# Performance work log

Hardware: AMD Instinct MI355X
Metric: run time of the kernel (lower is better)

The kernel has to match this reference:

```python
import jax, jax.numpy as jnp
import numpy as np

HIDDEN = 2048
N_HEADS = 16
HEAD_DIM = HIDDEN // N_HEADS
INV_NORM = 1.0 / float(np.sqrt(HEAD_DIM))
BETA = 1.0


def setup_inputs() -> dict:
    key = jax.random.key(0)
    ks = jax.random.split(key, 12)
    B, S, H = 2, 2048, HIDDEN
    scale = 1.0 / float(np.sqrt(H))
    return {
        "hidden_states": jax.random.normal(ks[0], (B, S, H), jnp.float32),
        "residual": jax.random.normal(ks[1], (B, S, H), jnp.float32),
        "alibi": jax.random.normal(ks[2], (B * N_HEADS, 1, S), jnp.float32),
        "Wq": jax.random.normal(ks[3], (H, H), jnp.float32) * scale,
        "bq": jnp.zeros((H,), jnp.float32),
        "Wk": jax.random.normal(ks[4], (H, H), jnp.float32) * scale,
        "bk": jnp.zeros((H,), jnp.float32),
        "Wv": jax.random.normal(ks[5], (H, H), jnp.float32) * scale,
        "bv": jnp.zeros((H,), jnp.float32),
        "Wd": jax.random.normal(ks[6], (H, H), jnp.float32) * scale,
        "bd": jnp.zeros((H,), jnp.float32),
    }


def reference(hidden_states, residual, alibi, Wq, bq, Wk, bk, Wv, bv, Wd, bd):
    B, S, H = hidden_states.shape
    # separate QKV projections (nn.Linear: x @ W^T + b)
    q = hidden_states @ Wq.T + bq
    k = hidden_states @ Wk.T + bk
    v = hidden_states @ Wv.T + bv
    # [B, n_heads, S, head_dim]
    q = q.reshape(B, S, N_HEADS, HEAD_DIM).transpose(0, 2, 1, 3)
    k = k.reshape(B, S, N_HEADS, HEAD_DIM).transpose(0, 2, 1, 3)
    v = v.reshape(B, S, N_HEADS, HEAD_DIM).transpose(0, 2, 1, 3)
    # baddbmm: scores = beta * alibi + inv_norm * q @ k^T, per (batch*head)
    alibi_bh = alibi.reshape(B, N_HEADS, 1, S)  # broadcasts over query dim
    scores = BETA * alibi_bh + INV_NORM * jnp.einsum("bhqd,bhkd->bhqk", q, k)
    probs = jax.nn.softmax(scores.astype(jnp.float32), axis=-1).astype(v.dtype)
    # attention dropout: p=0.0 (identity)
    ctx = jnp.einsum("bhqk,bhkd->bhqd", probs, v)  # [B,H,S,D]
    ctx = ctx.transpose(0, 2, 1, 3).reshape(B, S, H)
    out = ctx @ Wd.T + bd
    # hidden dropout p=0.0 then residual add (dropout_add)
    return out + residual
```

## Files before the change

kernel.cpp:

```cpp
#include <hip/hip_runtime.h>

#define HID   2048
#define NHEAD 16
#define HD    128
#define SEQ   2048
#define BATCH 2
#define MROWS (BATCH*SEQ)
#define NQKV  (3*HID)
#define INV_NORM 0.08838834764831845f
#define LOG2E    1.4426950408889634f
#define SCALE_L2 (INV_NORM*LOG2E)

typedef __attribute__((ext_vector_type(8)))  __bf16 bf16x8;
typedef __attribute__((ext_vector_type(4)))  float  f32x4;
typedef __attribute__((ext_vector_type(16))) float  f32x16;

typedef __attribute__((address_space(1))) void GV;
typedef __attribute__((address_space(3))) void LV;

__device__ __forceinline__ void async16(const void* g, void* l) {
  __builtin_amdgcn_global_load_lds((const GV*)g, (LV*)l, 16, 0, 0);
}

__device__ __forceinline__ unsigned short f2bf(float f) {
  unsigned u = __builtin_bit_cast(unsigned, f);
  u += 0x7FFFu + ((u >> 16) & 1u);
  return (unsigned short)(u >> 16);
}

__device__ __forceinline__ unsigned pkbf(float a, float b) {
#if __has_builtin(__builtin_amdgcn_cvt_pk_bf16_f32)
  typedef __attribute__((ext_vector_type(2))) __bf16 bf16x2;
  bf16x2 r = __builtin_amdgcn_cvt_pk_bf16_f32(a, b);
  return __builtin_bit_cast(unsigned, r);
#else
  return (unsigned)f2bf(a) | ((unsigned)f2bf(b) << 16);
#endif
}

__device__ __forceinline__ void mfma16(f32x4& c, bf16x8 a, bf16x8 b) {
  c = __builtin_amdgcn_mfma_f32_16x16x32_bf16(a, b, c, 0, 0, 0);
}

__global__ __launch_bounds__(256) void cvt_kernel(const float* __restrict__ src,
                                                  unsigned short* __restrict__ dst, int n) {
  int i = (blockIdx.x * 256 + threadIdx.x) * 4;
  if (i >= n) return;
  float4 v = *(const float4*)(src + i);
  ushort4 o;
  o.x = f2bf(v.x); o.y = f2bf(v.y); o.z = f2bf(v.z); o.w = f2bf(v.w);
  *(ushort4*)(dst + i) = o;
}

__global__ __launch_bounds__(256) void cvtw_kernel(const float* __restrict__ W0,
                                                   const float* __restrict__ W1,
                                                   const float* __restrict__ W2,
                                                   const float* __restrict__ W3,
                                                   unsigned short* __restrict__ dst) {
  int sel = blockIdx.y;
  const float* src = (sel == 0) ? W0 : (sel == 1) ? W1 : (sel == 2) ? W2 : W3;
  unsigned short* d = dst + (size_t)sel * HID * HID;
  int i = (blockIdx.x * 256 + threadIdx.x) * 4;
  float4 v = *(const float4*)(src + i);
  ushort4 o;
  o.x = f2bf(v.x); o.y = f2bf(v.y); o.z = f2bf(v.z); o.w = f2bf(v.w);
  *(ushort4*)(d + i) = o;
}

__device__ __forceinline__ void gemm_core(const unsigned short* __restrict__ A,
                                          const unsigned short* __restrict__ Bm,
                                          int K, int m0, int n0,
                                          unsigned short* As, unsigned short* Bs,
                                          f32x4 (&acc)[4][4]) {
  const int tid  = threadIdx.x;
  const int w    = tid >> 6;
  const int lane = tid & 63;
  const int l16  = lane & 15;
  const int quad = lane >> 4;
  const int wm   = (w & 1) * 64;
  const int wn   = (w >> 1) * 64;

  const f32x4 zero = {0.f, 0.f, 0.f, 0.f};
#pragma unroll
  for (int i = 0; i < 4; ++i)
#pragma unroll
    for (int j = 0; j < 4; ++j) acc[i][j] = zero;

  for (int k0 = 0; k0 < K; k0 += 64) {
    __syncthreads();
#pragma unroll
    for (int i = 0; i < 4; ++i) {
      int slot = i * 256 + w * 64 + lane;
      int r = slot >> 3;
      int c = (slot & 7) ^ (r & 7);
      async16(A  + (size_t)(m0 + r) * K + k0 + c * 8, (char*)As + (size_t)(i * 256 + w * 64) * 16);
      async16(Bm + (size_t)(n0 + r) * K + k0 + c * 8, (char*)Bs + (size_t)(i * 256 + w * 64) * 16);
    }
    __syncthreads();

#pragma unroll
    for (int kk = 0; kk < 2; ++kk) {
      bf16x8 af[4], bfp[4];
#pragma unroll
      for (int i = 0; i < 4; ++i) {
        int rr = wm + i * 16 + l16;
        af[i] = *(const bf16x8*)(As + ((rr * 8 + (((kk * 4 + quad)) ^ (rr & 7))) * 8));
      }
#pragma unroll
      for (int j = 0; j < 4; ++j) {
        int rr = wn + j * 16 + l16;
        bfp[j] = *(const bf16x8*)(Bs + ((rr * 8 + (((kk * 4 + quad)) ^ (rr & 7))) * 8));
      }
#pragma unroll
      for (int i = 0; i < 4; ++i)
#pragma unroll
        for (int j = 0; j < 4; ++j) mfma16(acc[i][j], af[i], bfp[j]);
    }
  }
}

__global__ __launch_bounds__(256) void gemm_qkv_kernel(
    const unsigned short* __restrict__ Xb, const unsigned short* __restrict__ Wb,
    const float* __restrict__ bq, const float* __restrict__ bk,
    const float* __restrict__ bv, unsigned short* __restrict__ Cout) {
  __shared__ __align__(16) unsigned short As[128 * 64];
  __shared__ __align__(16) unsigned short Bs[128 * 64];
  f32x4 acc[4][4];
  const int m0 = blockIdx.y * 128, n0 = blockIdx.x * 128;
  gemm_core(Xb, Wb, HID, m0, n0, As, Bs, acc);

  const int tid = threadIdx.x, w = tid >> 6, lane = tid & 63;
  const int l16 = lane & 15, quad = lane >> 4;
  const int wm = (w & 1) * 64, wn = (w >> 1) * 64;
#pragma unroll
  for (int j = 0; j < 4; ++j) {
    int ng = n0 + wn + j * 16 + l16;
    float bias = (ng < HID) ? bq[ng] : (ng < 2 * HID ? bk[ng - HID] : bv[ng - 2 * HID]);
#pragma unroll
    for (int i = 0; i < 4; ++i)
#pragma unroll
      for (int r = 0; r < 4; ++r) {
        int mg = m0 + wm + i * 16 + quad * 4 + r;
        Cout[(size_t)mg * NQKV + ng] = f2bf(acc[i][j][r] + bias);
      }
  }
}

__global__ __launch_bounds__(256) void gemm_out_kernel(
    const unsigned short* __restrict__ Ctx, const unsigned short* __restrict__ Wdb,
    const float* __restrict__ bd, const float* __restrict__ Res,
    float* __restrict__ Out) {
  __shared__ __align__(16) unsigned short As[128 * 64];
  __shared__ __align__(16) unsigned short Bs[128 * 64];
  f32x4 acc[4][4];
  const int m0 = blockIdx.y * 128, n0 = blockIdx.x * 128;
  gemm_core(Ctx, Wdb, HID, m0, n0, As, Bs, acc);

  const int tid = threadIdx.x, w = tid >> 6, lane = tid & 63;
  const int l16 = lane & 15, quad = lane >> 4;
  const int wm = (w & 1) * 64, wn = (w >> 1) * 64;
#pragma unroll
  for (int j = 0; j < 4; ++j) {
    int ng = n0 + wn + j * 16 + l16;
    float bias = bd[ng];
#pragma unroll
    for (int i = 0; i < 4; ++i)
#pragma unroll
      for (int r = 0; r < 4; ++r) {
        int mg = m0 + wm + i * 16 + quad * 4 + r;
        size_t off = (size_t)mg * HID + ng;
        Out[off] = acc[i][j][r] + bias + Res[off];
      }
  }
}

__global__ __launch_bounds__(256) void vtrans_kernel(const unsigned short* __restrict__ QKV,
                                                     unsigned short* __restrict__ Vt) {
  __shared__ __align__(16) unsigned short T[64][72];
  const int s0 = blockIdx.x * 64, d0 = blockIdx.y * 64, bh = blockIdx.z;
  const int b = bh >> 4, h = bh & 15;
  const int tid = threadIdx.x;
#pragma unroll
  for (int i = 0; i < 2; ++i) {
    int idx = i * 256 + tid;
    int r = idx >> 3, ch = idx & 7;
    const unsigned short* g = QKV + ((size_t)b * SEQ + s0 + r) * NQKV + 2 * HID + h * HD + d0 + ch * 8;
    *(uint4*)(&T[r][ch * 8]) = *(const uint4*)g;
  }
  __syncthreads();
#pragma unroll
  for (int i = 0; i < 2; ++i) {
    int idx = i * 256 + tid;
    int d = idx >> 3, ch = idx & 7;
    unsigned short v[8];
#pragma unroll
    for (int x = 0; x < 8; ++x) v[x] = T[ch * 8 + x][d];
    unsigned short* g = Vt + ((size_t)bh * HD + d0 + d) * SEQ + s0 + ch * 8;
    *(uint4*)g = *(const uint4*)v;
  }
}

__global__ __launch_bounds__(256, 2) void attn_kernel(
    const unsigned short* __restrict__ QKV, const unsigned short* __restrict__ Vt,
    const float* __restrict__ alibi, unsigned short* __restrict__ Ctx) {
  __shared__ __align__(16) char smem[51200];
  unsigned short* Ks  = (unsigned short*)smem;
  unsigned short* Vts = (unsigned short*)(smem + 16384);
  unsigned short* Ps  = (unsigned short*)(smem + 32768);
  unsigned short* Qs  = (unsigned short*)smem;

  const int tid = threadIdx.x, w = tid >> 6, lane = tid & 63;
  const int l32 = lane & 31, h = lane >> 5;
  const int q0 = blockIdx.x * 128;
  const int bh = blockIdx.y, b = bh >> 4, hh = bh & 15;
  const size_t rowbase = (size_t)b * SEQ;
  const float* ali = alibi + (size_t)bh * SEQ;
  const unsigned short* Vbh = Vt + (size_t)bh * HD * SEQ;

  {
    const unsigned short* qbase = QKV + (rowbase + q0) * NQKV + hh * HD;
#pragma unroll
    for (int i = 0; i < 8; ++i) {
      int slot = i * 256 + w * 64 + lane;
      int r = slot >> 4, c = (slot & 15) ^ (r & 15);
      async16(qbase + (size_t)r * NQKV + c * 8, (char*)Qs + (size_t)(i * 256 + w * 64) * 16);
    }
  }
  __syncthreads();
  bf16x8 qf[8];
  {
    int qr = w * 32 + l32;
#pragma unroll
    for (int ks = 0; ks < 8; ++ks) {
      int c = (ks * 2 + h) ^ (qr & 15);
      qf[ks] = *(const bf16x8*)(Qs + (qr * 16 + c) * 8);
    }
  }

  f32x16 oacc[4];
  float l_acc = 0.f;
#pragma unroll
  for (int nb = 0; nb < 4; ++nb)
#pragma unroll
    for (int r = 0; r < 16; ++r) oacc[nb][r] = 0.f;

  __syncthreads();

  for (int kt = 0; kt < SEQ / 64; ++kt) {
    {
      const unsigned short* kbase = QKV + (rowbase + kt * 64) * NQKV + HID + hh * HD;
#pragma unroll
      for (int i = 0; i < 4; ++i) {
        int slot = i * 256 + w * 64 + lane;
        int r = slot >> 4, c = (slot & 15) ^ (r & 15);
        async16(kbase + (size_t)r * NQKV + c * 8, (char*)Ks + (size_t)(i * 256 + w * 64) * 16);
      }
      const unsigned short* vbase = Vbh + kt * 64;
#pragma unroll
      for (int i = 0; i < 4; ++i) {
        int slot = i * 256 + w * 64 + lane;
        int r = slot >> 3, c = (slot & 7) ^ (r & 7);
        async16(vbase + (size_t)r * SEQ + c * 8, (char*)Vts + (size_t)(i * 256 + w * 64) * 16);
      }
    }
    __syncthreads();

    f32x16 sacc[2];
#pragma unroll
    for (int mb = 0; mb < 2; ++mb)
#pragma unroll
      for (int r = 0; r < 16; ++r) sacc[mb][r] = 0.f;
#pragma unroll
    for (int ks = 0; ks < 8; ++ks) {
      int c = (ks * 2 + h) ^ (l32 & 15);
#pragma unroll
      for (int mb = 0; mb < 2; ++mb) {
        bf16x8 kf = *(const bf16x8*)(Ks + ((mb * 32 + l32) * 16 + ((ks * 2 + h) ^ (l32 & 15))) * 8);
        sacc[mb] = __builtin_amdgcn_mfma_f32_32x32x16_bf16(kf, qf[ks], sacc[mb], 0, 0, 0);
      }
      (void)c;
    }

    const float* alik = ali + kt * 64 + 4 * h;
    const int qrow = w * 32 + l32;
#pragma unroll
    for (int mb = 0; mb < 2; ++mb) {
#pragma unroll
      for (int g = 0; g < 4; ++g) {
        float4 av = *(const float4*)(alik + mb * 32 + g * 8);
        float p0 = __builtin_amdgcn_exp2f(sacc[mb][g * 4 + 0] * SCALE_L2 + av.x * LOG2E);
        float p1 = __builtin_amdgcn_exp2f(sacc[mb][g * 4 + 1] * SCALE_L2 + av.y * LOG2E);
        float p2 = __builtin_amdgcn_exp2f(sacc[mb][g * 4 + 2] * SCALE_L2 + av.z * LOG2E);
        float p3 = __builtin_amdgcn_exp2f(sacc[mb][g * 4 + 3] * SCALE_L2 + av.w * LOG2E);
        l_acc += (p0 + p1) + (p2 + p3);
        uint2 pk;
        pk.x = pkbf(p0, p1);
        pk.y = pkbf(p2, p3);
        *(uint2*)(Ps + qrow * 72 + mb * 32 + g * 8 + 4 * h) = pk;
      }
    }

#pragma unroll
    for (int ks2 = 0; ks2 < 4; ++ks2) {
      bf16x8 pf = *(const bf16x8*)(Ps + qrow * 72 + ks2 * 16 + h * 8);
#pragma unroll
      for (int nb = 0; nb < 4; ++nb) {
        bf16x8 vf = *(const bf16x8*)(Vts + ((nb * 32 + l32) * 8 + ((ks2 * 2 + h) ^ (l32 & 7))) * 8);
        oacc[nb] = __builtin_amdgcn_mfma_f32_32x32x16_bf16(pf, vf, oacc[nb], 0, 0, 0);
      }
    }
    __syncthreads();
  }

  float lf = l_acc + __shfl_xor(l_acc, 32, 64);
  float rinv[16];
#pragma unroll
  for (int reg = 0; reg < 16; ++reg) {
    int row = (reg & 3) + 8 * (reg >> 2) + 4 * h;
    rinv[reg] = 1.0f / __shfl(lf, row, 64);
  }

#pragma unroll
  for (int nb = 0; nb < 4; ++nb)
#pragma unroll
    for (int reg = 0; reg < 16; ++reg) {
      int row = (reg & 3) + 8 * (reg >> 2) + 4 * h;
      size_t qg = rowbase + q0 + w * 32 + row;
      Ctx[qg * HID + hh * HD + nb * 32 + l32] = f2bf(oacc[nb][reg] * rinv[reg]);
    }
}

extern "C" void kernel_launch(void* const* d_in, const int* in_sizes, int n_in,
                              void* d_out, int out_size, void* d_ws, size_t ws_size,
                              hipStream_t stream) {
  const float* hidden   = (const float*)d_in[0];
  const float* residual = (const float*)d_in[1];
  const float* alibi    = (const float*)d_in[2];
  const float* Wq = (const float*)d_in[3];
  const float* bq = (const float*)d_in[4];
  const float* Wk = (const float*)d_in[5];
  const float* bk = (const float*)d_in[6];
  const float* Wv = (const float*)d_in[7];
  const float* bv = (const float*)d_in[8];
  const float* Wd = (const float*)d_in[9];
  const float* bd = (const float*)d_in[10];
  float* out = (float*)d_out;

  unsigned short* Xb    = (unsigned short*)d_ws;
  unsigned short* Wqkvb = Xb + (size_t)MROWS * HID;
  unsigned short* Wdb   = Wqkvb + (size_t)NQKV * HID;
  unsigned short* QKVb  = Wdb + (size_t)HID * HID;
  unsigned short* Ctxb  = QKVb + (size_t)MROWS * NQKV;
  unsigned short* Vtb   = Wqkvb;

  const int nX = MROWS * HID, nW = HID * HID;
  cvt_kernel<<<nX / 4 / 256, 256, 0, stream>>>(hidden, Xb, nX);
  cvtw_kernel<<<dim3(nW / 4 / 256, 4), 256, 0, stream>>>(Wq, Wk, Wv, Wd, Wqkvb);

  gemm_qkv_kernel<<<dim3(NQKV / 128, MROWS / 128), 256, 0, stream>>>(Xb, Wqkvb, bq, bk, bv, QKVb);
  vtrans_kernel<<<dim3(SEQ / 64, HD / 64, BATCH * NHEAD), 256, 0, stream>>>(QKVb, Vtb);
  attn_kernel<<<dim3(SEQ / 128, BATCH * NHEAD), 256, 0, stream>>>(QKVb, Vtb, alibi, Ctxb);
  gemm_out_kernel<<<dim3(HID / 128, MROWS / 128), 256, 0, stream>>>(Ctxb, Wdb, bd, residual, out);
}
```

Before: 442.1 us.

## Replace QKV GEMM with 256x256-tile, 8-wave, double-buffered ping-pong pipeline

The QKV projection GEMM moves from 128x128 tiles with 256 threads and a single LDS buffer to 256x256 tiles with 512 threads. The new kernel double-buffers A and B in LDS and splits each K step into eight phases that interleave async global->LDS loads with MFMA work, using barriers, explicit waitcnts and setprio. The block index is swizzled to improve L2 reuse of the operands. The aim is to hide load latency and raise arithmetic intensity, at the cost of more LDS (128 KB), higher register pressure and fragile hand-tuned synchronisation.

```diff
diff --git a/kernel.cpp b/kernel.cpp
--- a/kernel.cpp
+++ b/kernel.cpp
@@ -40,6 +40,10 @@
 
 __device__ __forceinline__ void mfma16(f32x4& c, bf16x8 a, bf16x8 b) {
   c = __builtin_amdgcn_mfma_f32_16x16x32_bf16(a, b, c, 0, 0, 0);
+}
+
+__device__ __forceinline__ bf16x8 frag(const unsigned short* buf, int row, int chunk) {
+  return *(const bf16x8*)(buf + ((row * 8 + (chunk ^ (row & 7))) << 3));
 }
 
 __global__ __launch_bounds__(256) void cvt_kernel(const float* __restrict__ src,
@@ -102,15 +106,9 @@
     for (int kk = 0; kk < 2; ++kk) {
       bf16x8 af[4], bfp[4];
 #pragma unroll
-      for (int i = 0; i < 4; ++i) {
-        int rr = wm + i * 16 + l16;
-        af[i] = *(const bf16x8*)(As + ((rr * 8 + (((kk * 4 + quad)) ^ (rr & 7))) * 8));
-      }
-#pragma unroll
-      for (int j = 0; j < 4; ++j) {
-        int rr = wn + j * 16 + l16;
-        bfp[j] = *(const bf16x8*)(Bs + ((rr * 8 + (((kk * 4 + quad)) ^ (rr & 7))) * 8));
-      }
+      for (int i = 0; i < 4; ++i) af[i]  = frag(As, wm + i * 16 + l16, kk * 4 + quad);
+#pragma unroll
+      for (int j = 0; j < 4; ++j) bfp[j] = frag(Bs, wn + j * 16 + l16, kk * 4 + quad);
 #pragma unroll
       for (int i = 0; i < 4; ++i)
 #pragma unroll
@@ -119,29 +117,209 @@
   }
 }
 
-__global__ __launch_bounds__(256) void gemm_qkv_kernel(
+#define ASZ (256 * 64)
+
+__global__ __launch_bounds__(512, 2) void gemm_qkv256_kernel(
     const unsigned short* __restrict__ Xb, const unsigned short* __restrict__ Wb,
     const float* __restrict__ bq, const float* __restrict__ bk,
     const float* __restrict__ bv, unsigned short* __restrict__ Cout) {
-  __shared__ __align__(16) unsigned short As[128 * 64];
-  __shared__ __align__(16) unsigned short Bs[128 * 64];
-  f32x4 acc[4][4];
-  const int m0 = blockIdx.y * 128, n0 = blockIdx.x * 128;
-  gemm_core(Xb, Wb, HID, m0, n0, As, Bs, acc);
-
-  const int tid = threadIdx.x, w = tid >> 6, lane = tid & 63;
-  const int l16 = lane & 15, quad = lane >> 4;
-  const int wm = (w & 1) * 64, wn = (w >> 1) * 64;
+  __shared__ __align__(16) unsigned short As[2 * ASZ];
+  __shared__ __align__(16) unsigned short Bs[2 * ASZ];
+
+  const int tid  = threadIdx.x;
+  const int w    = tid >> 6;
+  const int lane = tid & 63;
+  const int l16  = lane & 15;
+  const int quad = lane >> 4;
+  const int wm   = (w & 1) * 128;
+  const int wn   = (w >> 1) * 64;
+
+  const int wg = blockIdx.x;
+  const int sw = (wg & 7) * 48 + (wg >> 3);
+  const int m0 = (sw & 15) * 256;
+  const int n0 = (sw >> 4) * 256;
+
+  const unsigned short* Ag = Xb + (size_t)m0 * HID;
+  const unsigned short* Bg = Wb + (size_t)n0 * HID;
+
+  const int sr  = tid >> 3;
+  const int scs = ((tid & 7) ^ (sr & 7)) * 8;
+
+#define STG(SRC, DST, RB, KO)                                        \
+  async16((SRC) + (size_t)((RB) + sr) * HID + (KO) + scs,            \
+          (char*)(DST) + (((RB) * 8 + w * 64) * 16))
+
+  f32x4 acc[8][4];
+  const f32x4 zero = {0.f, 0.f, 0.f, 0.f};
+#pragma unroll
+  for (int a = 0; a < 8; ++a)
+#pragma unroll
+    for (int j = 0; j < 4; ++j) acc[a][j] = zero;
+
+  STG(Ag, As, 0, 0);  STG(Ag, As, 64, 0);  STG(Ag, As, 128, 0);  STG(Ag, As, 192, 0);
+  STG(Bg, Bs, 0, 0);  STG(Bg, Bs, 64, 0);  STG(Bg, Bs, 128, 0);  STG(Bg, Bs, 192, 0);
+  STG(Ag, As + ASZ, 0, 64);  STG(Ag, As + ASZ, 128, 64);
+  asm volatile("s_waitcnt vmcnt(2)" ::: "memory");
+  __builtin_amdgcn_s_barrier();
+
+  for (int i = 0; i < 16; ++i) {
+    const int k1 = (2 * i + 1) * 64;
+    const int t2 = 2 * i + 2, t3 = 2 * i + 3;
+    const int k2 = (t2 < 32 ? t2 : 31) * 64;
+    const int k3 = (t3 < 32 ? t3 : 31) * 64;
+    bf16x8 tb0[4], tb1[4];
+
+    {
+      bf16x8 ta[4];
+#pragma unroll
+      for (int ii = 0; ii < 4; ++ii) ta[ii] = frag(As, wm + ii * 16 + l16, quad);
+#pragma unroll
+      for (int j = 0; j < 4; ++j) tb0[j] = frag(Bs, wn + j * 16 + l16, quad);
+      STG(Ag, As + ASZ, 64, k1);
+      STG(Ag, As + ASZ, 192, k1);
+      __builtin_amdgcn_s_barrier();
+      asm volatile("s_waitcnt lgkmcnt(0)" ::: "memory");
+      __builtin_amdgcn_s_setprio(1);
+#pragma unroll
+      for (int ii = 0; ii < 4; ++ii)
+#pragma unroll
+        for (int j = 0; j < 4; ++j) mfma16(acc[ii][j], ta[ii], tb0[j]);
+      __builtin_amdgcn_s_setprio(0);
+      __builtin_amdgcn_s_barrier();
+    }
+    {
+      bf16x8 ta[4];
+#pragma unroll
+      for (int ii = 0; ii < 4; ++ii) ta[ii] = frag(As, wm + ii * 16 + l16, 4 + quad);
+#pragma unroll
+      for (int j = 0; j < 4; ++j) tb1[j] = frag(Bs, wn + j * 16 + l16, 4 + quad);
+      STG(Bg, Bs + ASZ, 0, k1);
+      STG(Bg, Bs + ASZ, 64, k1);
+      __builtin_amdgcn_s_barrier();
+      asm volatile("s_waitcnt lgkmcnt(0)" ::: "memory");
+      __builtin_amdgcn_s_setprio(1);
+#pragma unroll
+      for (int ii = 0; ii < 4; ++ii)
+#pragma unroll
+        for (int j = 0; j < 4; ++j) mfma16(acc[ii][j], ta[ii], tb1[j]);
+      __builtin_amdgcn_s_setprio(0);
+      __builtin_amdgcn_s_barrier();
+    }
+    {
+      bf16x8 ta[4];
+#pragma unroll
+      for (int ii = 0; ii < 4; ++ii) ta[ii] = frag(As, wm + 64 + ii * 16 + l16, quad);
+      STG(Bg, Bs + ASZ, 128, k1);
+      STG(Bg, Bs + ASZ, 192, k1);
+      __builtin_amdgcn_s_barrier();
+      asm volatile("s_waitcnt lgkmcnt(0)" ::: "memory");
+      __builtin_amdgcn_s_setprio(1);
+#pragma unroll
+      for (int ii = 0; ii < 4; ++ii)
+#pragma unroll
+        for (int j = 0; j < 4; ++j) mfma16(acc[4 + ii][j], ta[ii], tb0[j]);
+      __builtin_amdgcn_s_setprio(0);
+      __builtin_amdgcn_s_barrier();
+    }
+    {
+      bf16x8 ta[4];
+#pragma unroll
+      for (int ii = 0; ii < 4; ++ii) ta[ii] = frag(As, wm + 64 + ii * 16 + l16, 4 + quad);
+      STG(Ag, As, 0, k2);
+      STG(Ag, As, 128, k2);
+      __builtin_amdgcn_s_barrier();
+      asm volatile("s_waitcnt lgkmcnt(0)" ::: "memory");
+      __builtin_amdgcn_s_setprio(1);
+#pragma unroll
+      for (int ii = 0; ii < 4; ++ii)
+#pragma unroll
+        for (int j = 0; j < 4; ++j) mfma16(acc[4 + ii][j], ta[ii], tb1[j]);
+      __builtin_amdgcn_s_setprio(0);
+      asm volatile("s_waitcnt vmcnt(2)" ::: "memory");
+      __builtin_amdgcn_s_barrier();
+    }
+    {
+      bf16x8 ta[4];
+#pragma unroll
+      for (int ii = 0; ii < 4; ++ii) ta[ii] = frag(As + ASZ, wm + ii * 16 + l16, quad);
+#pragma unroll
+      for (int j = 0; j < 4; ++j) tb0[j] = frag(Bs + ASZ, wn + j * 16 + l16, quad);
+      STG(Ag, As, 64, k2);
+      STG(Ag, As, 192, k2);
+      __builtin_amdgcn_s_barrier();
+      asm volatile("s_waitcnt lgkmcnt(0)" ::: "memory");
+      __builtin_amdgcn_s_setprio(1);
+#pragma unroll
+      for (int ii = 0; ii < 4; ++ii)
+#pragma unroll
+        for (int j = 0; j < 4; ++j) mfma16(acc[ii][j], ta[ii], tb0[j]);
+      __builtin_amdgcn_s_setprio(0);
+      __builtin_amdgcn_s_barrier();
+    }
+    {
+      bf16x8 ta[4];
+#pragma unroll
+      for (int ii = 0; ii < 4; ++ii) ta[ii] = frag(As + ASZ, wm + ii * 16 + l16, 4 + quad);
+#pragma unroll
+      for (int j = 0; j < 4; ++j) tb1[j] = frag(Bs + ASZ, wn + j * 16 + l16, 4 + quad);
+      STG(Bg, Bs, 0, k2);
+      STG(Bg, Bs, 64, k2);
+      __builtin_amdgcn_s_barrier();
+      asm volatile("s_waitcnt lgkmcnt(0)" ::: "memory");
+      __builtin_amdgcn_s_setprio(1);
+#pragma unroll
+      for (int ii = 0; ii < 4; ++ii)
+#pragma unroll
+        for (int j = 0; j < 4; ++j) mfma16(acc[ii][j], ta[ii], tb1[j]);
+      __builtin_amdgcn_s_setprio(0);
+      __builtin_amdgcn_s_barrier();
+    }
+    {
+      bf16x8 ta[4];
+#pragma unroll
+      for (int ii = 0; ii < 4; ++ii) ta[ii] = frag(As + ASZ, wm + 64 + ii * 16 + l16, quad);
+      STG(Bg, Bs, 128, k2);
+      STG(Bg, Bs, 192, k2);
+      __builtin_amdgcn_s_barrier();
+      asm volatile("s_waitcnt lgkmcnt(0)" ::: "memory");
+      __builtin_amdgcn_s_setprio(1);
+#pragma unroll
+      for (int ii = 0; ii < 4; ++ii)
+#pragma unroll
+        for (int j = 0; j < 4; ++j) mfma16(acc[4 + ii][j], ta[ii], tb0[j]);
+      __builtin_amdgcn_s_setprio(0);
+      __builtin_amdgcn_s_barrier();
+    }
+    {
+      bf16x8 ta[4];
+#pragma unroll
+      for (int ii = 0; ii < 4; ++ii) ta[ii] = frag(As + ASZ, wm + 64 + ii * 16 + l16, 4 + quad);
+      STG(Ag, As + ASZ, 0, k3);
+      STG(Ag, As + ASZ, 128, k3);
+      __builtin_amdgcn_s_barrier();
+      asm volatile("s_waitcnt lgkmcnt(0)" ::: "memory");
+      __builtin_amdgcn_s_setprio(1);
+#pragma unroll
+      for (int ii = 0; ii < 4; ++ii)
+#pragma unroll
+        for (int j = 0; j < 4; ++j) mfma16(acc[4 + ii][j], ta[ii], tb1[j]);
+      __builtin_amdgcn_s_setprio(0);
+      asm volatile("s_waitcnt vmcnt(2)" ::: "memory");
+      __builtin_amdgcn_s_barrier();
+    }
+  }
+#undef STG
+
 #pragma unroll
   for (int j = 0; j < 4; ++j) {
     int ng = n0 + wn + j * 16 + l16;
     float bias = (ng < HID) ? bq[ng] : (ng < 2 * HID ? bk[ng - HID] : bv[ng - 2 * HID]);
 #pragma unroll
-    for (int i = 0; i < 4; ++i)
+    for (int a = 0; a < 8; ++a)
 #pragma unroll
       for (int r = 0; r < 4; ++r) {
-        int mg = m0 + wm + i * 16 + quad * 4 + r;
-        Cout[(size_t)mg * NQKV + ng] = f2bf(acc[i][j][r] + bias);
+        int mg = m0 + wm + (a >> 2) * 64 + (a & 3) * 16 + quad * 4 + r;
+        Cout[(size_t)mg * NQKV + ng] = f2bf(acc[a][j][r] + bias);
       }
   }
 }
@@ -272,13 +450,11 @@
       for (int r = 0; r < 16; ++r) sacc[mb][r] = 0.f;
 #pragma unroll
     for (int ks = 0; ks < 8; ++ks) {
-      int c = (ks * 2 + h) ^ (l32 & 15);
 #pragma unroll
       for (int mb = 0; mb < 2; ++mb) {
         bf16x8 kf = *(const bf16x8*)(Ks + ((mb * 32 + l32) * 16 + ((ks * 2 + h) ^ (l32 & 15))) * 8);
         sacc[mb] = __builtin_amdgcn_mfma_f32_32x32x16_bf16(kf, qf[ks], sacc[mb], 0, 0, 0);
       }
-      (void)c;
     }
 
     const float* alik = ali + kt * 64 + 4 * h;
@@ -357,7 +533,7 @@
   cvt_kernel<<<nX / 4 / 256, 256, 0, stream>>>(hidden, Xb, nX);
   cvtw_kernel<<<dim3(nW / 4 / 256, 4), 256, 0, stream>>>(Wq, Wk, Wv, Wd, Wqkvb);
 
-  gemm_qkv_kernel<<<dim3(NQKV / 128, MROWS / 128), 256, 0, stream>>>(Xb, Wqkvb, bq, bk, bv, QKVb);
+  gemm_qkv256_kernel<<<384, 512, 0, stream>>>(Xb, Wqkvb, bq, bk, bv, QKVb);
   vtrans_kernel<<<dim3(SEQ / 64, HD / 64, BATCH * NHEAD), 256, 0, stream>>>(QKVb, Vtb);
   attn_kernel<<<dim3(SEQ / 128, BATCH * NHEAD), 256, 0, stream>>>(QKVb, Vtb, alibi, Ctxb);
   gemm_out_kernel<<<dim3(HID / 128, MROWS / 128), 256, 0, stream>>>(Ctxb, Wdb, bd, residual, out);
```

Measured after the change: 454.4 us. +2.8%, slower.

## Replace QKV GEMM with triple-buffered 256x384 persistent-tile pipelined kernel

Applied to the files above, without the earlier changes.

Replaces the simple 128x128 QKV projection GEMM with a 512-thread kernel. Each workgroup holds a 256-row A slab and walks three 128-column B panels. A three-deep LDS ring overlaps async global-to-LDS loads with MFMA work, using explicit vmcnt waits, barriers and s_setprio. The grid is swizzled to 256 workgroups to improve L2 reuse of A and B. This targets load latency and synchronisation stalls in the single-buffered core, at the cost of more LDS per block and fragile manual wait-count bookkeeping.

```diff
diff --git a/kernel.cpp b/kernel.cpp
--- a/kernel.cpp
+++ b/kernel.cpp
@@ -40,6 +40,10 @@
 
 __device__ __forceinline__ void mfma16(f32x4& c, bf16x8 a, bf16x8 b) {
   c = __builtin_amdgcn_mfma_f32_16x16x32_bf16(a, b, c, 0, 0, 0);
+}
+
+__device__ __forceinline__ bf16x8 frag(const unsigned short* buf, int row, int chunk) {
+  return *(const bf16x8*)(buf + ((row * 8 + (chunk ^ (row & 7))) << 3));
 }
 
 __global__ __launch_bounds__(256) void cvt_kernel(const float* __restrict__ src,
@@ -102,15 +106,9 @@
     for (int kk = 0; kk < 2; ++kk) {
       bf16x8 af[4], bfp[4];
 #pragma unroll
-      for (int i = 0; i < 4; ++i) {
-        int rr = wm + i * 16 + l16;
-        af[i] = *(const bf16x8*)(As + ((rr * 8 + (((kk * 4 + quad)) ^ (rr & 7))) * 8));
-      }
-#pragma unroll
-      for (int j = 0; j < 4; ++j) {
-        int rr = wn + j * 16 + l16;
-        bfp[j] = *(const bf16x8*)(Bs + ((rr * 8 + (((kk * 4 + quad)) ^ (rr & 7))) * 8));
-      }
+      for (int i = 0; i < 4; ++i) af[i]  = frag(As, wm + i * 16 + l16, kk * 4 + quad);
+#pragma unroll
+      for (int j = 0; j < 4; ++j) bfp[j] = frag(Bs, wn + j * 16 + l16, kk * 4 + quad);
 #pragma unroll
       for (int i = 0; i < 4; ++i)
 #pragma unroll
@@ -119,31 +117,120 @@
   }
 }
 
-__global__ __launch_bounds__(256) void gemm_qkv_kernel(
+#define BUFU (24576)
+#define BUF3 (3 * BUFU)
+
+__global__ __launch_bounds__(512, 2) void gemm_qkv384_kernel(
     const unsigned short* __restrict__ Xb, const unsigned short* __restrict__ Wb,
     const float* __restrict__ bq, const float* __restrict__ bk,
     const float* __restrict__ bv, unsigned short* __restrict__ Cout) {
-  __shared__ __align__(16) unsigned short As[128 * 64];
-  __shared__ __align__(16) unsigned short Bs[128 * 64];
-  f32x4 acc[4][4];
-  const int m0 = blockIdx.y * 128, n0 = blockIdx.x * 128;
-  gemm_core(Xb, Wb, HID, m0, n0, As, Bs, acc);
-
-  const int tid = threadIdx.x, w = tid >> 6, lane = tid & 63;
-  const int l16 = lane & 15, quad = lane >> 4;
-  const int wm = (w & 1) * 64, wn = (w >> 1) * 64;
-#pragma unroll
-  for (int j = 0; j < 4; ++j) {
-    int ng = n0 + wn + j * 16 + l16;
-    float bias = (ng < HID) ? bq[ng] : (ng < 2 * HID ? bk[ng - HID] : bv[ng - 2 * HID]);
-#pragma unroll
-    for (int i = 0; i < 4; ++i)
-#pragma unroll
-      for (int r = 0; r < 4; ++r) {
-        int mg = m0 + wm + i * 16 + quad * 4 + r;
-        Cout[(size_t)mg * NQKV + ng] = f2bf(acc[i][j][r] + bias);
-      }
-  }
+  __shared__ __align__(16) unsigned short smem[BUF3];
+
+  const int tid  = threadIdx.x;
+  const int w    = tid >> 6;
+  const int lane = tid & 63;
+  const int l16  = lane & 15;
+  const int quad = lane >> 4;
+  const int wm   = (w & 1) * 128;
+  const int wn   = (w >> 1) * 32;
+
+  const int wg = blockIdx.x;
+  const int sw = (wg & 7) * 32 + (wg >> 3);
+  const int m0  = (sw & 15) * 256;
+  const int rn0 = (sw >> 4) * 384;
+
+  const unsigned short* Ag = Xb + (size_t)m0 * HID;
+
+  const int sr  = tid >> 3;
+  const int scs = ((tid & 7) ^ (sr & 7)) * 8;
+
+#define STGA(UB, RB, KT)                                              \
+  async16(Ag + (size_t)((RB) + sr) * HID + (KT) + scs,                \
+          (char*)smem + (size_t)(UB) * 2 + ((RB) * 8 + w * 64) * 16)
+#define STGB(UB, RB, KT)                                              \
+  async16(Bgp + (size_t)((RB) + sr) * HID + (KT) + scs,               \
+          (char*)smem + (size_t)(UB) * 2 + 32768 + ((RB) * 8 + w * 64) * 16)
+
+#define VM6  asm volatile("s_waitcnt vmcnt(6)" ::: "memory")
+#define VM0  asm volatile("s_waitcnt vmcnt(0)" ::: "memory")
+
+#define PHASE(UB, KK, STGBLK, WAITBLK)                                         \
+  {                                                                            \
+    const unsigned short* Ab = smem + (UB);                                    \
+    const unsigned short* Bb = Ab + 16384;                                     \
+    bf16x8 ta[8], tb[2];                                                       \
+    _Pragma("unroll")                                                          \
+    for (int ii = 0; ii < 8; ++ii) ta[ii] = frag(Ab, wm + ii * 16 + l16, (KK) * 4 + quad); \
+    _Pragma("unroll")                                                          \
+    for (int j = 0; j < 2; ++j)  tb[j] = frag(Bb, wn + j * 16 + l16, (KK) * 4 + quad);     \
+    STGBLK;                                                                    \
+    __builtin_amdgcn_s_barrier();                                              \
+    asm volatile("s_waitcnt lgkmcnt(0)" ::: "memory");                         \
+    __builtin_amdgcn_s_setprio(1);                                             \
+    _Pragma("unroll")                                                          \
+    for (int ii = 0; ii < 8; ++ii)                                             \
+      _Pragma("unroll")                                                        \
+      for (int j = 0; j < 2; ++j) mfma16(acc[ii][j], ta[ii], tb[j]);           \
+    __builtin_amdgcn_s_setprio(0);                                             \
+    WAITBLK;                                                                   \
+    __builtin_amdgcn_s_barrier();                                              \
+  }
+
+  for (int p = 0; p < 3; ++p) {
+    const unsigned short* Bgp = Wb + (size_t)(rn0 + p * 128) * HID;
+
+    f32x4 acc[8][2];
+    const f32x4 zero = {0.f, 0.f, 0.f, 0.f};
+#pragma unroll
+    for (int a = 0; a < 8; ++a) { acc[a][0] = zero; acc[a][1] = zero; }
+
+    STGA(0, 0, 0);  STGA(0, 64, 0);  STGA(0, 128, 0);  STGA(0, 192, 0);
+    STGB(0, 0, 0);  STGB(0, 64, 0);
+    STGA(BUFU, 0, 64);  STGA(BUFU, 64, 64);  STGA(BUFU, 128, 64);  STGA(BUFU, 192, 64);
+    STGB(BUFU, 0, 64);  STGB(BUFU, 64, 64);
+    VM6;
+    __builtin_amdgcn_s_barrier();
+
+    int ube = 0, ubo = BUFU;
+    int nbe = 2 * BUFU, nbo = 0;
+
+    for (int i = 0; i < 15; ++i) {
+      const int kpe = (2 * i + 2) * 64;
+      const int kpo = (2 * i + 3) * 64;
+
+      PHASE(ube, 0, { STGA(nbe, 0, kpe); STGA(nbe, 64, kpe); STGA(nbe, 128, kpe); }, {});
+      PHASE(ube, 1, { STGA(nbe, 192, kpe); STGB(nbe, 0, kpe); STGB(nbe, 64, kpe); }, VM6);
+      PHASE(ubo, 0, { STGA(nbo, 0, kpo); STGA(nbo, 64, kpo); STGA(nbo, 128, kpo); }, {});
+      PHASE(ubo, 1, { STGA(nbo, 192, kpo); STGB(nbo, 0, kpo); STGB(nbo, 64, kpo); }, VM6);
+
+      ube = nbe; ubo = nbo;
+      nbe = (nbe + 2 * BUFU >= BUF3) ? nbe + 2 * BUFU - BUF3 : nbe + 2 * BUFU;
+      nbo = (nbo + 2 * BUFU >= BUF3) ? nbo + 2 * BUFU - BUF3 : nbo + 2 * BUFU;
+    }
+
+    PHASE(ube, 0, {}, {});
+    PHASE(ube, 1, {}, VM0);
+    PHASE(ubo, 0, {}, {});
+    PHASE(ubo, 1, {}, {});
+
+#pragma unroll
+    for (int j = 0; j < 2; ++j) {
+      int ng = rn0 + p * 128 + wn + j * 16 + l16;
+      float bias = (ng < HID) ? bq[ng] : (ng < 2 * HID ? bk[ng - HID] : bv[ng - 2 * HID]);
+#pragma unroll
+      for (int a = 0; a < 8; ++a)
+#pragma unroll
+        for (int r = 0; r < 4; ++r) {
+          int mg = m0 + wm + a * 16 + quad * 4 + r;
+          Cout[(size_t)mg * NQKV + ng] = f2bf(acc[a][j][r] + bias);
+        }
+    }
+  }
+#undef STGA
+#undef STGB
+#undef PHASE
+#undef VM6
+#undef VM0
 }
 
 __global__ __launch_bounds__(256) void gemm_out_kernel(
@@ -272,13 +359,11 @@
       for (int r = 0; r < 16; ++r) sacc[mb][r] = 0.f;
 #pragma unroll
     for (int ks = 0; ks < 8; ++ks) {
-      int c = (ks * 2 + h) ^ (l32 & 15);
 #pragma unroll
       for (int mb = 0; mb < 2; ++mb) {
         bf16x8 kf = *(const bf16x8*)(Ks + ((mb * 32 + l32) * 16 + ((ks * 2 + h) ^ (l32 & 15))) * 8);
         sacc[mb] = __builtin_amdgcn_mfma_f32_32x32x16_bf16(kf, qf[ks], sacc[mb], 0, 0, 0);
       }
-      (void)c;
     }
 
     const float* alik = ali + kt * 64 + 4 * h;
@@ -357,7 +442,7 @@
   cvt_kernel<<<nX / 4 / 256, 256, 0, stream>>>(hidden, Xb, nX);
   cvtw_kernel<<<dim3(nW / 4 / 256, 4), 256, 0, stream>>>(Wq, Wk, Wv, Wd, Wqkvb);
 
-  gemm_qkv_kernel<<<dim3(NQKV / 128, MROWS / 128), 256, 0, stream>>>(Xb, Wqkvb, bq, bk, bv, QKVb);
+  gemm_qkv384_kernel<<<256, 512, 0, stream>>>(Xb, Wqkvb, bq, bk, bv, QKVb);
   vtrans_kernel<<<dim3(SEQ / 64, HD / 64, BATCH * NHEAD), 256, 0, stream>>>(QKVb, Vtb);
   attn_kernel<<<dim3(SEQ / 128, BATCH * NHEAD), 256, 0, stream>>>(QKVb, Vtb, alibi, Ctxb);
   gemm_out_kernel<<<dim3(HID / 128, MROWS / 128), 256, 0, stream>>>(Ctxb, Wdb, bd, residual, out);
```

New measurement: 449.0 us. About the same (+1.6%).
